# Performance work log

Measured on AMD Instinct MI355X. Metric: run time of the kernel, lower is better.

## Reference

```python
import jax, jax.numpy as jnp
import numpy as np

B, D_IN, H = 8192, 4096, 128
E, N, C = 3, 256, 32          # experts, codebook_size, codebook_dim
D1, D2 = 512, 256             # down_units
U1, U2 = 256, 512             # up_units
CW = 0.25                     # commitment_weight


def setup_inputs() -> dict:
    key = jax.random.key(0)
    ks = jax.random.split(key, 16)
    s = 0.02
    f32 = jnp.float32
    inp = {
        'x':   jax.random.normal(ks[0], (B, D_IN), f32),
        # llm_down MLP: 4096 -> 512 -> 256 -> 128 (ReLU on hiddens, linear out)
        'Wd1': jax.random.normal(ks[1], (D_IN, D1), f32) * s, 'bd1': jnp.zeros((D1,), f32),
        'Wd2': jax.random.normal(ks[2], (D1, D2), f32) * s,  'bd2': jnp.zeros((D2,), f32),
        'Wd3': jax.random.normal(ks[3], (D2, H), f32) * s,   'bd3': jnp.zeros((H,), f32),
        # per-expert VQ: project_in 128->32, codebook [256,32], project_out 32->128
        'Win':  jax.random.normal(ks[4], (E, H, C), f32) * s, 'bin_': jnp.zeros((E, C), f32),
        'codebook': jax.random.normal(ks[5], (E, N, C), f32),
        'Wout': jax.random.normal(ks[6], (E, C, H), f32) * s, 'bout': jnp.zeros((E, H), f32),
        # llm_up MLP: 128 -> 256 -> 512 -> 4096
        'Wu1': jax.random.normal(ks[7], (H, U1), f32) * s,   'bu1': jnp.zeros((U1,), f32),
        'Wu2': jax.random.normal(ks[8], (U1, U2), f32) * s,  'bu2': jnp.zeros((U2,), f32),
        'Wu3': jax.random.normal(ks[9], (U2, D_IN), f32) * s, 'bu3': jnp.zeros((D_IN,), f32),
    }
    return inp


def _decorrelation_loss(qemb):
    # qemb: [B, E, H]
    b, e, h = qemb.shape
    cen = qemb - qemb.mean(axis=0, keepdims=True)
    cen = cen.transpose(1, 0, 2).reshape(e, -1)          # [E, B*H]
    cov = (cen @ cen.T) / (b * h - 1)                    # [E, E]
    std = jnp.sqrt(jnp.diag(cov))
    std = jnp.where(std > 1e-8, std, 1.0)
    corr = cov / jnp.outer(std, std)
    c2 = corr ** 2
    return c2.sum() - jnp.diag(c2).sum()


def _vq_experts(latent, Win, bin_, codebook, Wout, bout):
    # latent: [B,H]; all experts share the same (unmasked) latent.
    xe = jnp.einsum('bh,ehc->ebc', latent, Win) + bin_[:, None, :]      # [E,B,C]
    d2 = ((xe ** 2).sum(-1)[..., None]
          - 2.0 * jnp.einsum('ebc,enc->ebn', xe, codebook)
          + (codebook ** 2).sum(-1)[:, None, :])                        # [E,B,N]
    idx = jnp.argmin(d2, axis=-1)                                       # [E,B]
    q = jax.vmap(lambda c, i: c[i])(codebook, idx)                      # [E,B,C] gather
    commit = CW * jnp.mean((jax.lax.stop_gradient(q) - xe) ** 2, axis=(1, 2)).sum()
    quant = xe + jax.lax.stop_gradient(q - xe)                          # straight-through
    qe = jnp.einsum('ebc,ech->ebh', quant, Wout) + bout[:, None, :]     # [E,B,H]
    return qe, idx, commit


def reference(x, Wd1, bd1, Wd2, bd2, Wd3, bd3, Win, bin_, codebook, Wout, bout,
              Wu1, bu1, Wu2, bu2, Wu3, bu3):
    h = jax.nn.relu(x @ Wd1 + bd1)
    h = jax.nn.relu(h @ Wd2 + bd2)
    latent = h @ Wd3 + bd3                                              # [B,128]
    qe, idx, total_commit = _vq_experts(latent, Win, bin_, codebook, Wout, bout)
    qemb = qe.transpose(1, 0, 2)                                        # [B,E,H]
    decorr = _decorrelation_loss(qemb)
    rl = qemb.mean(axis=1)                                              # [B,H]
    u = jax.nn.relu(rl @ Wu1 + bu1)
    u = jax.nn.relu(u @ Wu2 + bu2)
    recon = jnp.clip(u @ Wu3 + bu3, -1.0, 1.0)                          # [B,4096]
    return (recon, idx.T, total_commit, decorr)
```

## Files before the change

### kernel.cpp

```cpp
#include <hip/hip_runtime.h>
#include <hip/hip_bf16.h>

using bf16 = __hip_bfloat16;

typedef __bf16 bf16x8 __attribute__((ext_vector_type(8)));
typedef float  f32x4  __attribute__((ext_vector_type(4)));
typedef unsigned int u32x4 __attribute__((ext_vector_type(4)));
typedef unsigned long long u64;
typedef unsigned short u16;
typedef unsigned int u32;

__device__ __forceinline__ float b2f(bf16 v) { return __bfloat162float(v); }
__device__ __forceinline__ bf16  f2b(float v) { return __float2bfloat16(v); }
__device__ __forceinline__ u16   bits(bf16 v) { return __builtin_bit_cast(u16, v); }

static constexpr size_t SZ_WD1S = 512ull  * 8192  * 2;
static constexpr size_t SZ_WD2S = 256ull  * 1536  * 2;
static constexpr size_t SZ_WFUS = 128ull  * 768   * 2;
static constexpr size_t SZ_WU1T = 256ull  * 128   * 2;
static constexpr size_t SZ_WU2T = 512ull  * 256   * 2;
static constexpr size_t SZ_WU3T = 4096ull * 512   * 2;
static constexpr size_t SZ_H1S  = 8192ull * 1536  * 2;
static constexpr size_t SZ_H2S  = 8192ull * 768   * 2;
static constexpr size_t SZ_XE   = 8192ull * 128   * 4;
static constexpr size_t SZ_QEMB = 3ull * 8192 * 128 * 4;
static constexpr size_t SZ_RL   = 8192ull * 128   * 2;
static constexpr size_t SZ_U1   = 8192ull * 256   * 2;
static constexpr size_t SZ_U2   = 8192ull * 512   * 2;
static constexpr size_t SZ_CNRM = 768ull * 4;
static constexpr size_t SZ_BFUS = 128ull * 4;
static constexpr size_t SZ_PART = 4ull * 8192 * 512 * 4;

static constexpr size_t OFF_WD1S = 0;
static constexpr size_t OFF_WD2S = OFF_WD1S + SZ_WD1S;
static constexpr size_t OFF_WFUS = OFF_WD2S + SZ_WD2S;
static constexpr size_t OFF_WU1T = OFF_WFUS + SZ_WFUS;
static constexpr size_t OFF_WU2T = OFF_WU1T + SZ_WU1T;
static constexpr size_t OFF_WU3T = OFF_WU2T + SZ_WU2T;
static constexpr size_t OFF_H1S  = OFF_WU3T + SZ_WU3T;
static constexpr size_t OFF_H2S  = OFF_H1S  + SZ_H1S;
static constexpr size_t OFF_XE   = OFF_H2S  + SZ_H2S;
static constexpr size_t OFF_QEMB = OFF_XE   + SZ_XE;
static constexpr size_t OFF_RL   = OFF_QEMB + SZ_QEMB;
static constexpr size_t OFF_U1   = OFF_RL   + SZ_RL;
static constexpr size_t OFF_U2   = OFF_U1   + SZ_U1;
static constexpr size_t OFF_CNRM = OFF_U2   + SZ_U2;
static constexpr size_t OFF_BFUS = OFF_CNRM + ((SZ_CNRM + 255) & ~size_t(255));
static constexpr size_t OFF_STAT = OFF_BFUS + ((SZ_BFUS + 255) & ~size_t(255));
static constexpr size_t OFF_PART = OFF_STAT + 2048;

__global__ void wtrans_bf16(const float* __restrict__ in, bf16* __restrict__ out,
                            int K, int N)
{
    __shared__ float tile[32][33];
    const int tx = threadIdx.x, ty = threadIdx.y;
    const int n0 = blockIdx.x * 32, k0 = blockIdx.y * 32;
    #pragma unroll
    for (int i = 0; i < 32; i += 8)
        tile[ty + i][tx] = in[(size_t)(k0 + ty + i) * N + n0 + tx];
    __syncthreads();
    #pragma unroll
    for (int i = 0; i < 32; i += 8)
        out[(size_t)(n0 + ty + i) * K + k0 + tx] = f2b(tile[tx][ty + i]);
}

__global__ void wtrans_split3(const float* __restrict__ in, bf16* __restrict__ out,
                              int K, int N)
{
    __shared__ float tile[32][33];
    const int tx = threadIdx.x, ty = threadIdx.y;
    const int n0 = blockIdx.x * 32, k0 = blockIdx.y * 32;
    #pragma unroll
    for (int i = 0; i < 32; i += 8)
        tile[ty + i][tx] = in[(size_t)(k0 + ty + i) * N + n0 + tx];
    __syncthreads();
    #pragma unroll
    for (int i = 0; i < 32; i += 8) {
        const float v = tile[tx][ty + i];
        const bf16 hi = f2b(v);
        const bf16 lo = f2b(v - b2f(hi));
        bf16* o = out + (size_t)(n0 + ty + i) * 3 * K + 3 * (k0 + tx);
        o[0] = hi; o[1] = lo; o[2] = hi;
    }
}

__global__ void wtrans_hilo(const float* __restrict__ in, bf16* __restrict__ out,
                            int K, int N)
{
    __shared__ float tile[32][33];
    const int tx = threadIdx.x, ty = threadIdx.y;
    const int n0 = blockIdx.x * 32, k0 = blockIdx.y * 32;
    #pragma unroll
    for (int i = 0; i < 32; i += 8)
        tile[ty + i][tx] = in[(size_t)(k0 + ty + i) * N + n0 + tx];
    __syncthreads();
    const int kg = k0 >> 5;
    #pragma unroll
    for (int i = 0; i < 32; i += 8) {
        const float v = tile[tx][ty + i];
        const bf16 hi = f2b(v);
        const bf16 lo = f2b(v - b2f(hi));
        bf16* o = out + (size_t)(n0 + ty + i) * 8192 + kg * 64 + tx;
        o[0] = hi; o[32] = lo;
    }
}

__global__ void cnorm_kernel(const float* __restrict__ cb, float* __restrict__ cnorm)
{
    const int i = blockIdx.x * blockDim.x + threadIdx.x;
    if (i < 768) {
        float s = 0.f;
        for (int k = 0; k < 32; ++k) { const float v = cb[i * 32 + k]; s += v * v; }
        cnorm[i] = s;
    }
}

__global__ __launch_bounds__(256)
void wfuse_kernel(const float* __restrict__ Wd3, const float* __restrict__ bd3,
                  const float* __restrict__ Win, const float* __restrict__ bin_,
                  bf16* __restrict__ BtS, float* __restrict__ bfuse)
{
    const int n = blockIdx.x;
    const int t = threadIdx.x;
    if (n >= 96) {
        bf16* o = BtS + (size_t)n * 768 + 3 * t;
        o[0] = f2b(0.f); o[1] = f2b(0.f); o[2] = f2b(0.f);
        if (t == 0) bfuse[n] = 0.f;
        return;
    }
    const int e = n >> 5, c = n & 31;
    float s = 0.f;
    for (int h = 0; h < 128; ++h)
        s += Wd3[t * 128 + h] * Win[(size_t)(e * 128 + h) * 32 + c];
    const bf16 hi = f2b(s);
    const bf16 lo = f2b(s - b2f(hi));
    bf16* o = BtS + (size_t)n * 768 + 3 * t;
    o[0] = hi; o[1] = lo; o[2] = hi;
    if (t == 0) {
        float b = bin_[e * 32 + c];
        for (int h = 0; h < 128; ++h)
            b += bd3[h] * Win[(size_t)(e * 128 + h) * 32 + c];
        bfuse[n] = b;
    }
}

__global__ __launch_bounds__(256, 4)
void gemm1_x3(const float* __restrict__ A, const bf16* __restrict__ Bhl,
              float* __restrict__ part)
{
    __shared__ bf16 As[128 * 64];
    __shared__ bf16 Bs[128 * 64];
    const int t = threadIdx.x, lane = t & 63, w = t >> 6;
    const int bid = blockIdx.x + blockIdx.y * 4 + blockIdx.z * 256;
    const int xcd = bid & 7, j = bid >> 3;
    const int panel = xcd + 8 * (j >> 6);
    const int n0 = (panel & 3) * 128;
    const int kz = panel >> 2;
    const int m0 = (j & 63) * 128;
    const int wr = w >> 1, wc = w & 1, l15 = lane & 15, quad = lane >> 4;
    const int offh = ((quad ^ (l15 & 7)) << 3);
    const int offl = offh ^ 32;

    f32x4 acc[4][4];
    #pragma unroll
    for (int i = 0; i < 4; ++i)
        #pragma unroll
        for (int jj = 0; jj < 4; ++jj)
            #pragma unroll
            for (int rr = 0; rr < 4; ++rr) acc[i][jj][rr] = 0.f;

    const int arow = t >> 1, ahalf = t & 1, arx = arow & 7;
    bf16* const aw0 = As + arow * 64 + (((ahalf * 2 + 0) ^ arx) << 3);
    bf16* const aw1 = As + arow * 64 + (((ahalf * 2 + 1) ^ arx) << 3);
    bf16* const aw2 = As + arow * 64 + (((4 + ahalf * 2 + 0) ^ arx) << 3);
    bf16* const aw3 = As + arow * 64 + (((4 + ahalf * 2 + 1) ^ arx) << 3);

    int brow[4], bco[4];
    #pragma unroll
    for (int i = 0; i < 4; ++i) {
        const int p = i * 256 + t;
        brow[i] = p >> 3;
        bco[i] = ((p & 7) ^ (brow[i] & 7)) * 8;
    }

    const int s0 = kz * 32, s1 = s0 + 32;
    const float* const apbase = A + (size_t)(m0 + arow) * 4096 + ahalf * 16;

    float f[16];
    {
        const float* ap = apbase + s0 * 32;
        *(float4*)(f + 0)  = *(const float4*)(ap + 0);
        *(float4*)(f + 4)  = *(const float4*)(ap + 4);
        *(float4*)(f + 8)  = *(const float4*)(ap + 8);
        *(float4*)(f + 12) = *(const float4*)(ap + 12);
    }

    for (int ks = s0; ks < s1; ++ks) {
        const bool haveNext = (ks + 1 < s1);
        #pragma unroll
        for (int i = 0; i < 4; ++i) {
            const bf16* gb = Bhl + (size_t)(n0 + brow[i]) * 8192 + ks * 64 + bco[i];
            __builtin_amdgcn_global_load_lds(
                (const __attribute__((address_space(1))) void*)gb,
                (__attribute__((address_space(3))) void*)(Bs + (size_t)(i * 256 + t) * 8), 16, 0, 0);
        }
        float g[16];
        if (haveNext) {
            const float* ap = apbase + (ks + 1) * 32;
            *(float4*)(g + 0)  = *(const float4*)(ap + 0);
            *(float4*)(g + 4)  = *(const float4*)(ap + 4);
            *(float4*)(g + 8)  = *(const float4*)(ap + 8);
            *(float4*)(g + 12) = *(const float4*)(ap + 12);
        }
        {
            u32x4 hv, lv;
            #pragma unroll
            for (int jj = 0; jj < 4; ++jj) {
                const bf16 h0 = f2b(f[2 * jj]), h1 = f2b(f[2 * jj + 1]);
                const u32 l0 = bits(f2b(f[2 * jj] - b2f(h0)));
                const u32 l1 = bits(f2b(f[2 * jj + 1] - b2f(h1)));
                hv[jj] = (u32)bits(h0) | ((u32)bits(h1) << 16);
                lv[jj] = l0 | (l1 << 16);
            }
            *(u32x4*)aw0 = hv; *(u32x4*)aw2 = lv;
            #pragma unroll
            for (int jj = 0; jj < 4; ++jj) {
                const bf16 h0 = f2b(f[8 + 2 * jj]), h1 = f2b(f[8 + 2 * jj + 1]);
                const u32 l0 = bits(f2b(f[8 + 2 * jj] - b2f(h0)));
                const u32 l1 = bits(f2b(f[8 + 2 * jj + 1] - b2f(h1)));
                hv[jj] = (u32)bits(h0) | ((u32)bits(h1) << 16);
                lv[jj] = l0 | (l1 << 16);
            }
            *(u32x4*)aw1 = hv; *(u32x4*)aw3 = lv;
        }
        __syncthreads();
        {
            bf16x8 ah[4], al[4];
            #pragma unroll
            for (int mi = 0; mi < 4; ++mi) {
                const bf16* ar = As + (wr * 64 + mi * 16 + l15) * 64;
                ah[mi] = *(const bf16x8*)(ar + offh);
                al[mi] = *(const bf16x8*)(ar + offl);
            }
            #pragma unroll
            for (int ni = 0; ni < 4; ++ni) {
                const bf16* br = Bs + (wc * 64 + ni * 16 + l15) * 64;
                const bf16x8 bh = *(const bf16x8*)(br + offh);
                const bf16x8 bl = *(const bf16x8*)(br + offl);
                #pragma unroll
                for (int mi = 0; mi < 4; ++mi) {
                    acc[mi][ni] = __builtin_amdgcn_mfma_f32_16x16x32_bf16(ah[mi], bh, acc[mi][ni], 0, 0, 0);
                    acc[mi][ni] = __builtin_amdgcn_mfma_f32_16x16x32_bf16(al[mi], bh, acc[mi][ni], 0, 0, 0);
                    acc[mi][ni] = __builtin_amdgcn_mfma_f32_16x16x32_bf16(ah[mi], bl, acc[mi][ni], 0, 0, 0);
                }
            }
        }
        __syncthreads();
        if (haveNext) {
            #pragma unroll
            for (int k = 0; k < 16; ++k) f[k] = g[k];
        }
    }

    float* op = part + (size_t)kz * (8192ull * 512);
    #pragma unroll
    for (int mi = 0; mi < 4; ++mi)
        #pragma unroll
        for (int ni = 0; ni < 4; ++ni) {
            const int col = n0 + wc * 64 + ni * 16 + l15;
            #pragma unroll
            for (int rr = 0; rr < 4; ++rr) {
                const int row = m0 + wr * 64 + mi * 16 + quad * 4 + rr;
                op[(size_t)row * 512 + col] = acc[mi][ni][rr];
            }
        }
}

__global__ __launch_bounds__(256)
void h1_epi(const float* __restrict__ part, const float* __restrict__ bias,
            bf16* __restrict__ out)
{
    const int idx = blockIdx.x * 256 + threadIdx.x;
    const int r = idx >> 7, c4 = idx & 127;
    const size_t base = (size_t)r * 512 + c4 * 4;
    const float4 p0 = *(const float4*)(part + 0ull * 8192 * 512 + base);
    const float4 p1 = *(const float4*)(part + 1ull * 8192 * 512 + base);
    const float4 p2 = *(const float4*)(part + 2ull * 8192 * 512 + base);
    const float4 p3 = *(const float4*)(part + 3ull * 8192 * 512 + base);
    const float4 bv = *(const float4*)(bias + c4 * 4);
    float v[4];
    v[0] = p0.x + p1.x + p2.x + p3.x + bv.x;
    v[1] = p0.y + p1.y + p2.y + p3.y + bv.y;
    v[2] = p0.z + p1.z + p2.z + p3.z + bv.z;
    v[3] = p0.w + p1.w + p2.w + p3.w + bv.w;
    u64 h[4], l[4];
    #pragma unroll
    for (int j = 0; j < 4; ++j) {
        const float vv = v[j] > 0.f ? v[j] : 0.f;
        const bf16 hi = f2b(vv);
        h[j] = bits(hi);
        l[j] = bits(f2b(vv - b2f(hi)));
    }
    const u64 w0 = h[0] | (h[0] << 16) | (l[0] << 32) | (h[1] << 48);
    const u64 w1 = h[1] | (l[1] << 16) | (h[2] << 32) | (h[2] << 48);
    const u64 w2 = l[2] | (h[3] << 16) | (h[3] << 32) | (l[3] << 48);
    u64* dst = (u64*)(out + (size_t)r * 1536 + 12 * c4);
    dst[0] = w0; dst[1] = w1; dst[2] = w2;
}

template <int EPI, int RELU, int BM>
__global__ __launch_bounds__(256)
void gemm_bt(const bf16* __restrict__ A, const bf16* __restrict__ Bt,
             const float* __restrict__ bias, void* __restrict__ outp,
             int M, int N, int K)
{
    constexpr int MI = BM / 32;
    __shared__ bf16 As[BM * 64];
    __shared__ bf16 Bs[128 * 64];
    const int t = threadIdx.x, lane = t & 63, w = t >> 6;
    const int n0 = blockIdx.x * 128;
    const int m0 = blockIdx.y * BM;
    const int wr = w >> 1, wc = w & 1, l15 = lane & 15, quad = lane >> 4;
    const int l7 = l15 & 7;

    f32x4 acc[MI][4];
    #pragma unroll
    for (int i = 0; i < MI; ++i)
        #pragma unroll
        for (int j = 0; j < 4; ++j)
            #pragma unroll
            for (int r = 0; r < 4; ++r) acc[i][j][r] = 0.f;

    for (int k0 = 0; k0 < K; k0 += 64) {
        #pragma unroll
        for (int i = 0; i < 4; ++i) {
            const int c = i * 256 + t;
            const int row = c >> 3;
            const int col = ((c & 7) ^ (row & 7)) * 8;
            const bf16* gb = Bt + (size_t)(n0 + row) * K + k0 + col;
            __builtin_amdgcn_global_load_lds(
                (const __attribute__((address_space(1))) void*)gb,
                (__attribute__((address_space(3))) void*)(Bs + (size_t)c * 8), 16, 0, 0);
            if (i < BM / 32) {
                const bf16* ga = A + (size_t)(m0 + row) * K + k0 + col;
                __builtin_amdgcn_global_load_lds(
                    (const __attribute__((address_space(1))) void*)ga,
                    (__attribute__((address_space(3))) void*)(As + (size_t)c * 8), 16, 0, 0);
            }
        }
        __syncthreads();
        #pragma unroll
        for (int kk = 0; kk < 2; ++kk) {
            const int sw = (((kk << 2) | quad) ^ l7) << 3;
            bf16x8 af[MI], bfr[4];
            #pragma unroll
            for (int mi = 0; mi < MI; ++mi)
                af[mi] = *(const bf16x8*)(As + (wr * (BM / 2) + mi * 16 + l15) * 64 + sw);
            #pragma unroll
            for (int ni = 0; ni < 4; ++ni)
                bfr[ni] = *(const bf16x8*)(Bs + (wc * 64 + ni * 16 + l15) * 64 + sw);
            #pragma unroll
            for (int mi = 0; mi < MI; ++mi)
                #pragma unroll
                for (int ni = 0; ni < 4; ++ni)
                    acc[mi][ni] = __builtin_amdgcn_mfma_f32_16x16x32_bf16(
                        af[mi], bfr[ni], acc[mi][ni], 0, 0, 0);
        }
        __syncthreads();
    }

    #pragma unroll
    for (int mi = 0; mi < MI; ++mi)
        #pragma unroll
        for (int ni = 0; ni < 4; ++ni) {
            const int col = n0 + wc * 64 + ni * 16 + l15;
            const float bv = bias[col];
            #pragma unroll
            for (int r = 0; r < 4; ++r) {
                const int row = m0 + wr * (BM / 2) + mi * 16 + quad * 4 + r;
                float v = acc[mi][ni][r] + bv;
                if (RELU) v = v > 0.f ? v : 0.f;
                if (EPI == 0) {
                    ((float*)outp)[(size_t)row * N + col] = v;
                } else if (EPI == 1) {
                    const bf16 hi = f2b(v);
                    const bf16 lo = f2b(v - b2f(hi));
                    bf16* o = (bf16*)outp + (size_t)row * 3 * N + 3 * col;
                    o[0] = hi; o[1] = hi; o[2] = lo;
                } else if (EPI == 2) {
                    ((bf16*)outp)[(size_t)row * N + col] = f2b(v);
                } else {
                    v = fminf(fmaxf(v, -1.f), 1.f);
                    ((float*)outp)[(size_t)row * N + col] = v;
                }
            }
        }
}

__global__ __launch_bounds__(256)
void vq2_kernel(const float* __restrict__ xe_buf, const float* __restrict__ cb,
                const float* __restrict__ cnorm, const float* __restrict__ Wout,
                const float* __restrict__ bout, float* __restrict__ qemb,
                float* __restrict__ idx_out, float* __restrict__ commit_acc)
{
    __shared__ float cb_s[256 * 36];
    __shared__ float wo_s[32 * 128];
    __shared__ float cn_s[256];
    __shared__ float bo_s[128];
    __shared__ float xe_s[4 * 32];
    __shared__ float q_s[4 * 32];
    __shared__ int   idx_s[4];
    __shared__ u64   wred[4][4];
    __shared__ float cred[256];

    const int e  = blockIdx.x >> 8;
    const int rb = blockIdx.x & 255;
    const int t = threadIdx.x, lane = t & 63, w = t >> 6;

    for (int j = t; j < 256 * 32; j += 256) {
        const int code = j >> 5, c = j & 31;
        cb_s[code * 36 + c] = cb[(size_t)e * 8192 + j];
    }
    for (int j = t; j < 4096; j += 256) wo_s[j] = Wout[(size_t)e * 4096 + j];
    cn_s[t] = cnorm[e * 256 + t];
    if (t < 128) bo_s[t] = bout[e * 128 + t];
    float commit_loc = 0.f;
    __syncthreads();

    for (int it = 0; it < 8; ++it) {
        const int r0 = rb * 32 + it * 4;
        if (t < 128) {
            const int r4 = t >> 5, c = t & 31;
            xe_s[r4 * 32 + c] = xe_buf[(size_t)(r0 + r4) * 128 + e * 32 + c];
        }
        __syncthreads();

        u64 key[4];
        {
            const float4* cp = (const float4*)(cb_s + t * 36);
            const float cn = cn_s[t];
            #pragma unroll
            for (int r4 = 0; r4 < 4; ++r4) {
                float dot = 0.f;
                #pragma unroll
                for (int c4 = 0; c4 < 8; ++c4) {
                    const float4 cv = cp[c4];
                    const float4 xv = *(const float4*)(xe_s + r4 * 32 + c4 * 4);
                    dot += xv.x * cv.x + xv.y * cv.y + xv.z * cv.z + xv.w * cv.w;
                }
                const float d = cn - 2.f * dot;
                u32 ub = __builtin_bit_cast(u32, d);
                ub = (ub & 0x80000000u) ? ~ub : (ub | 0x80000000u);
                key[r4] = ((u64)ub << 32) | (u32)t;
            }
        }
        #pragma unroll
        for (int off = 32; off; off >>= 1) {
            #pragma unroll
            for (int r4 = 0; r4 < 4; ++r4) {
                const u64 o = __shfl_down(key[r4], off, 64);
                if (o < key[r4]) key[r4] = o;
            }
        }
        if (lane == 0) {
            #pragma unroll
            for (int r4 = 0; r4 < 4; ++r4) wred[r4][w] = key[r4];
        }
        __syncthreads();
        if (t < 4) {
            u64 k = wred[t][0];
            #pragma unroll
            for (int ww = 1; ww < 4; ++ww) if (wred[t][ww] < k) k = wred[t][ww];
            const int code = (int)(k & 0xFFFFFFFFu);
            idx_s[t] = code;
            idx_out[(size_t)(r0 + t) * 3 + e] = (float)code;
        }
        __syncthreads();
        if (t < 128) {
            const int r4 = t >> 5, c = t & 31;
            const float q = cb_s[idx_s[r4] * 36 + c];
            q_s[r4 * 32 + c] = q;
            const float dd = q - xe_s[r4 * 32 + c];
            commit_loc += dd * dd;
        }
        __syncthreads();
        #pragma unroll
        for (int p = 0; p < 2; ++p) {
            const int j = p * 256 + t;
            const int r4 = j >> 7, h = j & 127;
            float s = bo_s[h];
            #pragma unroll
            for (int c = 0; c < 32; ++c) s += q_s[r4 * 32 + c] * wo_s[c * 128 + h];
            qemb[((size_t)e * 8192 + r0 + r4) * 128 + h] = s;
        }
        __syncthreads();
    }

    cred[t] = commit_loc;
    __syncthreads();
    for (int o = 128; o; o >>= 1) { if (t < o) cred[t] += cred[t + o]; __syncthreads(); }
    if (t == 0) atomicAdd(commit_acc, cred[0]);
}

__global__ __launch_bounds__(256)
void rlmean_kernel(const float* __restrict__ qemb, bf16* __restrict__ rl,
                   float* __restrict__ meanAcc)
{
    const int t = threadIdx.x, h = t & 127, half = t >> 7;
    const int r0 = blockIdx.x * 64;
    float a0 = 0.f, a1 = 0.f, a2 = 0.f;
    for (int r = r0 + half; r < r0 + 64; r += 2) {
        const float v0 = qemb[((size_t)0 * 8192 + r) * 128 + h];
        const float v1 = qemb[((size_t)1 * 8192 + r) * 128 + h];
        const float v2 = qemb[((size_t)2 * 8192 + r) * 128 + h];
        a0 += v0; a1 += v1; a2 += v2;
        rl[(size_t)r * 128 + h] = f2b((v0 + v1 + v2) * (1.f / 3.f));
    }
    __shared__ float red[3][256];
    red[0][t] = a0; red[1][t] = a1; red[2][t] = a2;
    __syncthreads();
    if (t < 128) {
        atomicAdd(&meanAcc[0 * 128 + h], red[0][t] + red[0][t + 128]);
        atomicAdd(&meanAcc[1 * 128 + h], red[1][t] + red[1][t + 128]);
        atomicAdd(&meanAcc[2 * 128 + h], red[2][t] + red[2][t + 128]);
    }
}

__global__ __launch_bounds__(256)
void gram_kernel(const float* __restrict__ qemb, const float* __restrict__ meanAcc,
                 double* __restrict__ gram)
{
    const int t = threadIdx.x;
    const int h = t & 127, half = t >> 7;
    const int b0 = blockIdx.x * 32;
    const float m0 = meanAcc[0 * 128 + h] * (1.f / 8192.f);
    const float m1 = meanAcc[1 * 128 + h] * (1.f / 8192.f);
    const float m2 = meanAcc[2 * 128 + h] * (1.f / 8192.f);
    float g[6] = {0, 0, 0, 0, 0, 0};
    for (int b = b0 + half; b < b0 + 32; b += 2) {
        const float v0 = qemb[((size_t)0 * 8192 + b) * 128 + h] - m0;
        const float v1 = qemb[((size_t)1 * 8192 + b) * 128 + h] - m1;
        const float v2 = qemb[((size_t)2 * 8192 + b) * 128 + h] - m2;
        g[0] += v0 * v0; g[1] += v0 * v1; g[2] += v0 * v2;
        g[3] += v1 * v1; g[4] += v1 * v2; g[5] += v2 * v2;
    }
    __shared__ float red[256];
    for (int i = 0; i < 6; ++i) {
        red[t] = g[i];
        __syncthreads();
        for (int o = 128; o; o >>= 1) { if (t < o) red[t] += red[t + o]; __syncthreads(); }
        if (t == 0) atomicAdd(&gram[i], (double)red[0]);
        __syncthreads();
    }
}

__global__ void final_kernel(const float* __restrict__ commit_acc,
                             const double* __restrict__ gram,
                             float* __restrict__ out2)
{
    if (threadIdx.x != 0 || blockIdx.x != 0) return;
    const double denom = 8192.0 * 128.0 - 1.0;
    const double c00 = gram[0] / denom, c01 = gram[1] / denom, c02 = gram[2] / denom;
    const double c11 = gram[3] / denom, c12 = gram[4] / denom, c22 = gram[5] / denom;
    double s0 = sqrt(c00), s1 = sqrt(c11), s2 = sqrt(c22);
    if (!(s0 > 1e-8)) s0 = 1.0;
    if (!(s1 > 1e-8)) s1 = 1.0;
    if (!(s2 > 1e-8)) s2 = 1.0;
    const double r01 = c01 / (s0 * s1), r02 = c02 / (s0 * s2), r12 = c12 / (s1 * s2);
    const double decorr = 2.0 * (r01 * r01 + r02 * r02 + r12 * r12);
    out2[0] = (float)((double)commit_acc[0] * (0.25 / (8192.0 * 32.0)));
    out2[1] = (float)decorr;
}

extern "C" void kernel_launch(void* const* d_in, const int* in_sizes, int n_in,
                              void* d_out, int out_size, void* d_ws, size_t ws_size,
                              hipStream_t stream)
{
    const float* x    = (const float*)d_in[0];
    const float* Wd1  = (const float*)d_in[1];
    const float* bd1  = (const float*)d_in[2];
    const float* Wd2  = (const float*)d_in[3];
    const float* bd2  = (const float*)d_in[4];
    const float* Wd3  = (const float*)d_in[5];
    const float* bd3  = (const float*)d_in[6];
    const float* Win  = (const float*)d_in[7];
    const float* bin_ = (const float*)d_in[8];
    const float* cb   = (const float*)d_in[9];
    const float* Wout = (const float*)d_in[10];
    const float* bout = (const float*)d_in[11];
    const float* Wu1  = (const float*)d_in[12];
    const float* bu1  = (const float*)d_in[13];
    const float* Wu2  = (const float*)d_in[14];
    const float* bu2  = (const float*)d_in[15];
    const float* Wu3  = (const float*)d_in[16];
    const float* bu3  = (const float*)d_in[17];

    char* ws = (char*)d_ws;
    bf16*  Wd1s   = (bf16*)(ws + OFF_WD1S);
    bf16*  Wd2s   = (bf16*)(ws + OFF_WD2S);
    bf16*  WfuseS = (bf16*)(ws + OFF_WFUS);
    bf16*  Wu1T   = (bf16*)(ws + OFF_WU1T);
    bf16*  Wu2T   = (bf16*)(ws + OFF_WU2T);
    bf16*  Wu3T   = (bf16*)(ws + OFF_WU3T);
    bf16*  h1s    = (bf16*)(ws + OFF_H1S);
    bf16*  h2s    = (bf16*)(ws + OFF_H2S);
    float* xe     = (float*)(ws + OFF_XE);
    float* qemb   = (float*)(ws + OFF_QEMB);
    bf16*  rl     = (bf16*)(ws + OFF_RL);
    bf16*  u1     = (bf16*)(ws + OFF_U1);
    bf16*  u2     = (bf16*)(ws + OFF_U2);
    float* cnorm  = (float*)(ws + OFF_CNRM);
    float* bfuse  = (float*)(ws + OFF_BFUS);
    float* commit = (float*)(ws + OFF_STAT);
    double* gram  = (double*)(ws + OFF_STAT + 8);
    float* meanA  = (float*)(ws + OFF_STAT + 64);
    float* part   = (float*)(ws + OFF_PART);

    float* out_f   = (float*)d_out;
    float* idx_out = out_f + (size_t)8192 * 4096;
    float* scal    = idx_out + (size_t)8192 * 3;

    hipMemsetAsync(ws + OFF_STAT, 0, 2048, stream);

    const dim3 tb(32, 8);
    wtrans_hilo<<<dim3(16, 128), tb, 0, stream>>>(Wd1, Wd1s, 4096, 512);
    wtrans_split3<<<dim3(8, 16),   tb, 0, stream>>>(Wd2, Wd2s, 512, 256);
    wtrans_bf16<<<dim3(8, 4),      tb, 0, stream>>>(Wu1, Wu1T, 128, 256);
    wtrans_bf16<<<dim3(16, 8),     tb, 0, stream>>>(Wu2, Wu2T, 256, 512);
    wtrans_bf16<<<dim3(128, 16),   tb, 0, stream>>>(Wu3, Wu3T, 512, 4096);
    cnorm_kernel<<<3, 256, 0, stream>>>(cb, cnorm);
    wfuse_kernel<<<128, 256, 0, stream>>>(Wd3, bd3, Win, bin_, WfuseS, bfuse);

    gemm1_x3<<<dim3(4, 64, 4), 256, 0, stream>>>(x, Wd1s, part);
    h1_epi<<<4096, 256, 0, stream>>>(part, bd1, h1s);
    gemm_bt<1, 1, 64><<<dim3(2, 128), 256, 0, stream>>>(h1s, Wd2s, bd2, h2s, 8192, 256, 1536);
    gemm_bt<0, 0, 64><<<dim3(1, 128), 256, 0, stream>>>(h2s, WfuseS, bfuse, xe, 8192, 128, 768);

    vq2_kernel<<<768, 256, 0, stream>>>(xe, cb, cnorm, Wout, bout, qemb, idx_out, commit);
    rlmean_kernel<<<128, 256, 0, stream>>>(qemb, rl, meanA);
    gram_kernel<<<256, 256, 0, stream>>>(qemb, meanA, gram);
    final_kernel<<<1, 64, 0, stream>>>(commit, gram, scal);

    gemm_bt<2, 1, 64><<<dim3(2, 128),  256, 0, stream>>>(rl, Wu1T, bu1, u1,    8192, 256,  128);
    gemm_bt<2, 1, 64><<<dim3(4, 128),  256, 0, stream>>>(u1, Wu2T, bu2, u2,    8192, 512,  256);
    gemm_bt<3, 0, 128><<<dim3(32, 64), 256, 0, stream>>>(u2, Wu3T, bu3, out_f, 8192, 4096, 512);

    (void)in_sizes; (void)n_in; (void)out_size; (void)ws_size;
}
```

Baseline: 654.7 us.

## Fuse gram with mean pass via raw moments; drop A-prefetch in gemm1

Merges the row-mean and gram kernels into one pass that accumulates raw cross-products, and applies the mean correction afterwards in the final scalar kernel. This removes a second full read of qemb and one kernel launch. Separately, gemm1 no longer prefetches the next A slice into registers and loads it at the top of each iteration instead, which lowers register pressure but exposes load latency. Using raw second moments in float risks more cancellation error in the decorrelation loss.

```diff
diff --git a/kernel.cpp b/kernel.cpp
--- a/kernel.cpp
+++ b/kernel.cpp
@@ -184,33 +184,19 @@
     }
 
     const int s0 = kz * 32, s1 = s0 + 32;
-    const float* const apbase = A + (size_t)(m0 + arow) * 4096 + ahalf * 16;
-
-    float f[16];
-    {
-        const float* ap = apbase + s0 * 32;
+    for (int ks = s0; ks < s1; ++ks) {
+        const float* ap = A + (size_t)(m0 + arow) * 4096 + ks * 32 + ahalf * 16;
+        float f[16];
         *(float4*)(f + 0)  = *(const float4*)(ap + 0);
         *(float4*)(f + 4)  = *(const float4*)(ap + 4);
         *(float4*)(f + 8)  = *(const float4*)(ap + 8);
         *(float4*)(f + 12) = *(const float4*)(ap + 12);
-    }
-
-    for (int ks = s0; ks < s1; ++ks) {
-        const bool haveNext = (ks + 1 < s1);
         #pragma unroll
         for (int i = 0; i < 4; ++i) {
             const bf16* gb = Bhl + (size_t)(n0 + brow[i]) * 8192 + ks * 64 + bco[i];
             __builtin_amdgcn_global_load_lds(
                 (const __attribute__((address_space(1))) void*)gb,
                 (__attribute__((address_space(3))) void*)(Bs + (size_t)(i * 256 + t) * 8), 16, 0, 0);
-        }
-        float g[16];
-        if (haveNext) {
-            const float* ap = apbase + (ks + 1) * 32;
-            *(float4*)(g + 0)  = *(const float4*)(ap + 0);
-            *(float4*)(g + 4)  = *(const float4*)(ap + 4);
-            *(float4*)(g + 8)  = *(const float4*)(ap + 8);
-            *(float4*)(g + 12) = *(const float4*)(ap + 12);
         }
         {
             u32x4 hv, lv;
@@ -256,10 +242,6 @@
             }
         }
         __syncthreads();
-        if (haveNext) {
-            #pragma unroll
-            for (int k = 0; k < 16; ++k) f[k] = g[k];
-        }
     }
 
     float* op = part + (size_t)kz * (8192ull * 512);
@@ -503,47 +485,31 @@
 }
 
 __global__ __launch_bounds__(256)
-void rlmean_kernel(const float* __restrict__ qemb, bf16* __restrict__ rl,
-                   float* __restrict__ meanAcc)
+void rlgram_kernel(const float* __restrict__ qemb, bf16* __restrict__ rl,
+                   float* __restrict__ meanAcc, double* __restrict__ gram)
 {
     const int t = threadIdx.x, h = t & 127, half = t >> 7;
-    const int r0 = blockIdx.x * 64;
+    const int r0 = blockIdx.x * 32;
     float a0 = 0.f, a1 = 0.f, a2 = 0.f;
-    for (int r = r0 + half; r < r0 + 64; r += 2) {
+    float g[6] = {0, 0, 0, 0, 0, 0};
+    for (int r = r0 + half; r < r0 + 32; r += 2) {
         const float v0 = qemb[((size_t)0 * 8192 + r) * 128 + h];
         const float v1 = qemb[((size_t)1 * 8192 + r) * 128 + h];
         const float v2 = qemb[((size_t)2 * 8192 + r) * 128 + h];
         a0 += v0; a1 += v1; a2 += v2;
+        g[0] += v0 * v0; g[1] += v0 * v1; g[2] += v0 * v2;
+        g[3] += v1 * v1; g[4] += v1 * v2; g[5] += v2 * v2;
         rl[(size_t)r * 128 + h] = f2b((v0 + v1 + v2) * (1.f / 3.f));
     }
-    __shared__ float red[3][256];
-    red[0][t] = a0; red[1][t] = a1; red[2][t] = a2;
+    __shared__ float red3[3][256];
+    red3[0][t] = a0; red3[1][t] = a1; red3[2][t] = a2;
     __syncthreads();
     if (t < 128) {
-        atomicAdd(&meanAcc[0 * 128 + h], red[0][t] + red[0][t + 128]);
-        atomicAdd(&meanAcc[1 * 128 + h], red[1][t] + red[1][t + 128]);
-        atomicAdd(&meanAcc[2 * 128 + h], red[2][t] + red[2][t + 128]);
-    }
-}
-
-__global__ __launch_bounds__(256)
-void gram_kernel(const float* __restrict__ qemb, const float* __restrict__ meanAcc,
-                 double* __restrict__ gram)
-{
-    const int t = threadIdx.x;
-    const int h = t & 127, half = t >> 7;
-    const int b0 = blockIdx.x * 32;
-    const float m0 = meanAcc[0 * 128 + h] * (1.f / 8192.f);
-    const float m1 = meanAcc[1 * 128 + h] * (1.f / 8192.f);
-    const float m2 = meanAcc[2 * 128 + h] * (1.f / 8192.f);
-    float g[6] = {0, 0, 0, 0, 0, 0};
-    for (int b = b0 + half; b < b0 + 32; b += 2) {
-        const float v0 = qemb[((size_t)0 * 8192 + b) * 128 + h] - m0;
-        const float v1 = qemb[((size_t)1 * 8192 + b) * 128 + h] - m1;
-        const float v2 = qemb[((size_t)2 * 8192 + b) * 128 + h] - m2;
-        g[0] += v0 * v0; g[1] += v0 * v1; g[2] += v0 * v2;
-        g[3] += v1 * v1; g[4] += v1 * v2; g[5] += v2 * v2;
-    }
+        atomicAdd(&meanAcc[0 * 128 + h], red3[0][t] + red3[0][t + 128]);
+        atomicAdd(&meanAcc[1 * 128 + h], red3[1][t] + red3[1][t + 128]);
+        atomicAdd(&meanAcc[2 * 128 + h], red3[2][t] + red3[2][t + 128]);
+    }
+    __syncthreads();
     __shared__ float red[256];
     for (int i = 0; i < 6; ++i) {
         red[t] = g[i];
@@ -556,12 +522,25 @@
 
 __global__ void final_kernel(const float* __restrict__ commit_acc,
                              const double* __restrict__ gram,
+                             const float* __restrict__ meanAcc,
                              float* __restrict__ out2)
 {
     if (threadIdx.x != 0 || blockIdx.x != 0) return;
+    double corr[6] = {0, 0, 0, 0, 0, 0};
+    for (int h = 0; h < 128; ++h) {
+        const double m0 = meanAcc[0 * 128 + h];
+        const double m1 = meanAcc[1 * 128 + h];
+        const double m2 = meanAcc[2 * 128 + h];
+        corr[0] += m0 * m0; corr[1] += m0 * m1; corr[2] += m0 * m2;
+        corr[3] += m1 * m1; corr[4] += m1 * m2; corr[5] += m2 * m2;
+    }
     const double denom = 8192.0 * 128.0 - 1.0;
-    const double c00 = gram[0] / denom, c01 = gram[1] / denom, c02 = gram[2] / denom;
-    const double c11 = gram[3] / denom, c12 = gram[4] / denom, c22 = gram[5] / denom;
+    const double c00 = (gram[0] - corr[0] / 8192.0) / denom;
+    const double c01 = (gram[1] - corr[1] / 8192.0) / denom;
+    const double c02 = (gram[2] - corr[2] / 8192.0) / denom;
+    const double c11 = (gram[3] - corr[3] / 8192.0) / denom;
+    const double c12 = (gram[4] - corr[4] / 8192.0) / denom;
+    const double c22 = (gram[5] - corr[5] / 8192.0) / denom;
     double s0 = sqrt(c00), s1 = sqrt(c11), s2 = sqrt(c22);
     if (!(s0 > 1e-8)) s0 = 1.0;
     if (!(s1 > 1e-8)) s1 = 1.0;
@@ -637,9 +616,8 @@
     gemm_bt<0, 0, 64><<<dim3(1, 128), 256, 0, stream>>>(h2s, WfuseS, bfuse, xe, 8192, 128, 768);
 
     vq2_kernel<<<768, 256, 0, stream>>>(xe, cb, cnorm, Wout, bout, qemb, idx_out, commit);
-    rlmean_kernel<<<128, 256, 0, stream>>>(qemb, rl, meanA);
-    gram_kernel<<<256, 256, 0, stream>>>(qemb, meanA, gram);
-    final_kernel<<<1, 64, 0, stream>>>(commit, gram, scal);
+    rlgram_kernel<<<256, 256, 0, stream>>>(qemb, rl, meanA, gram);
+    final_kernel<<<1, 64, 0, stream>>>(commit, gram, meanA, scal);
 
     gemm_bt<2, 1, 64><<<dim3(2, 128),  256, 0, stream>>>(rl, Wu1T, bu1, u1,    8192, 256,  128);
     gemm_bt<2, 1, 64><<<dim3(4, 128),  256, 0, stream>>>(u1, Wu2T, bu2, u2,    8192, 512,  256);
```

Measured after the change: 566.6 us. 13.5% less time.
